# Kernel optimization log

Hardware: AMD Instinct MI355X
Metric: run time of the kernel (lower is better)

The kernel has to match this reference:

```python
import jax, jax.numpy as jnp
from jax import lax
import numpy as np

B, C, T = 512, 12, 4096
DS = 4          # int_downsize
STEPS = 7       # int_steps
KS = 51         # smooth_size
SIGMA = (KS - 1) // 2  # 25, per module: gaussian_filter1d(delta, smooth_centre)


def _gauss_kernel():
    # Replicates scipy.ndimage.gaussian_filter1d(delta, SIGMA) on a length-KS
    # delta array with default truncate=4.0 and mode='reflect'.
    r = int(4.0 * SIGMA + 0.5)
    x = np.arange(-r, r + 1)
    g = np.exp(-0.5 * (x / SIGMA) ** 2)
    g /= g.sum()
    delta = np.zeros(KS)
    delta[(KS - 1) // 2] = 1.0
    padded = np.pad(delta, r, mode='symmetric')  # scipy 'reflect' boundary
    filt = np.convolve(padded, g, mode='valid')  # len == KS (g is symmetric)
    return filt.astype(np.float32)


def resize_linear(x, factor):
    # F.interpolate(mode='linear', align_corners=False, recompute_scale_factor=False)
    Tin = x.shape[-1]
    Tout = int(Tin * factor)
    src = (jnp.arange(Tout, dtype=x.dtype) + 0.5) / factor - 0.5
    src = jnp.clip(src, 0.0, Tin - 1)
    i0 = jnp.floor(src).astype(jnp.int32)
    i1 = jnp.minimum(i0 + 1, Tin - 1)
    w = src - i0
    return x[..., i0] * (1.0 - w) + x[..., i1] * w


def resize_transform(x, factor):
    # ResizeTransformTime: resize the field AND rescale its magnitude
    if factor < 1:
        return factor * resize_linear(x, factor)
    elif factor > 1:
        return resize_linear(factor * x, factor)
    return x


def warp_1d(src, flow):
    # SpatialTransformer for 1D signals: torch fakes 2D grid_sample by repeating
    # src to [B,C,Tlen,2] and the grid to [B,1,Tlen,2]; with align_corners=True,
    # zeros padding, bilinear. The width-dim (size 2) interpolation collapses to a
    # scalar in-bounds weight xw since both width copies are identical.
    Tlen = src.shape[-1]
    new_locs = jnp.arange(Tlen, dtype=src.dtype) + flow          # [B,1,Tlen]
    v = 2.0 * (new_locs / (Tlen - 1) - 0.5)                      # normalized
    ix = (v + 1.0) * 0.5                                         # W=2 -> (W-1)=1
    iy = (v + 1.0) * 0.5 * (Tlen - 1)
    x0 = jnp.floor(ix)
    fx = ix - x0
    x0i = x0.astype(jnp.int32)
    xw = ((1.0 - fx) * ((x0i >= 0) & (x0i <= 1))
          + fx * ((x0i + 1 >= 0) & (x0i + 1 <= 1)))              # [B,1,Tlen]
    y0 = jnp.floor(iy)
    fy = iy - y0
    y0i = y0.astype(jnp.int32)
    y1i = y0i + 1
    vy0 = (y0i >= 0) & (y0i < Tlen)
    vy1 = (y1i >= 0) & (y1i < Tlen)
    y0c = jnp.clip(y0i, 0, Tlen - 1)
    y1c = jnp.clip(y1i, 0, Tlen - 1)
    Bc, Cc = src.shape[0], src.shape[1]
    idx0 = jnp.broadcast_to(y0c, (Bc, Cc, Tlen))
    idx1 = jnp.broadcast_to(y1c, (Bc, Cc, Tlen))
    g0 = jnp.take_along_axis(src, idx0, axis=-1)
    g1 = jnp.take_along_axis(src, idx1, axis=-1)
    return xw * ((1.0 - fy) * vy0 * g0 + fy * vy1 * g1)


def setup_inputs() -> dict:
    key = jax.random.key(0)
    k1, k2 = jax.random.split(key)
    source = jax.random.normal(k1, (B, C, T), dtype=jnp.float32)
    noise = jax.random.normal(k2, (B, 1, T), dtype=jnp.float32)
    flow_mag = jnp.ones((1,), dtype=jnp.float32)
    smooth_kernel = jnp.asarray(_gauss_kernel())
    return {"source": source, "flow_mag": flow_mag, "noise": noise,
            "smooth_kernel": smooth_kernel}


def reference(source, flow_mag, noise, smooth_kernel):
    flow_field = flow_mag * noise                      # [B,1,T]
    pos_flow = resize_transform(flow_field, 1.0 / DS)  # [B,1,T//DS]
    # VecInt: scaling and squaring
    vec = pos_flow * (1.0 / 2 ** STEPS)
    for _ in range(STEPS):
        vec = vec + warp_1d(vec, vec)
    pos_flow = resize_transform(vec, float(DS))        # back to [B,1,T]
    # conv1d smoothing (cross-correlation, same as F.conv1d)
    pad = (KS - 1) // 2
    pos_flow = lax.conv_general_dilated(
        pos_flow, smooth_kernel.reshape(1, 1, KS),
        window_strides=(1,), padding=[(pad, pad)],
        dimension_numbers=('NCH', 'OIH', 'NCH'))
    return warp_1d(source, pos_flow)
```

## Files before the change

kernel.cpp:

```cpp
#include <hip/hip_runtime.h>


#define BB 512
#define CC 12
#define TT 4096
#define TD 1024
#define KS 51
#define NT 1024

struct WarpW { int y0c, y1c; float w0, w1; };

template <int TLEN>
__device__ __forceinline__ WarpW warp_weights(int t, float flow) {
    const float tm1 = (float)(TLEN - 1);
    float nl = (float)t + flow;
    float v  = 2.0f * (nl / tm1 - 0.5f);
    float ix = (v + 1.0f) * 0.5f;
    float iy = ix * tm1;
    float x0 = floorf(ix);
    float fx = ix - x0;
    int   x0i = (int)x0;
    float m0 = (x0i >= 0 && x0i <= 1) ? 1.0f : 0.0f;
    float m1 = (x0i + 1 >= 0 && x0i + 1 <= 1) ? 1.0f : 0.0f;
    float xw = (1.0f - fx) * m0 + fx * m1;
    float y0 = floorf(iy);
    float fy = iy - y0;
    int   y0i = (int)y0;
    int   y1i = y0i + 1;
    float vy0 = (y0i >= 0 && y0i < TLEN) ? 1.0f : 0.0f;
    float vy1 = (y1i >= 0 && y1i < TLEN) ? 1.0f : 0.0f;
    WarpW r;
    r.y0c = min(max(y0i, 0), TLEN - 1);
    r.y1c = min(max(y1i, 0), TLEN - 1);
    r.w0 = xw * (1.0f - fy) * vy0;
    r.w1 = xw * fy * vy1;
    return r;
}

extern "C" __global__ void __launch_bounds__(NT)
rand_warp_aug_kernel(const float* __restrict__ source,
                     const float* __restrict__ flow_mag,
                     const float* __restrict__ noise,
                     const float* __restrict__ gk,
                     float* __restrict__ out) {
    __shared__ float vecA[TD];
    __shared__ float vecB[TD];
    __shared__ float pf_up[TT];
    __shared__ float g[KS];

    const int b   = blockIdx.x;
    const int tid = threadIdx.x;
    const float fm = flow_mag[0];

    const float* nrow = noise + (size_t)b * TT;
    if (tid < TD) {
        float x1 = fm * nrow[4 * tid + 1];
        float x2 = fm * nrow[4 * tid + 2];
        vecA[tid] = (x1 * 0.5f + x2 * 0.5f) * (0.25f * 0.0078125f);
    }
    if (tid < KS) g[tid] = gk[tid];
    __syncthreads();

    float* cur = vecA;
    float* nxt = vecB;
#pragma unroll 1
    for (int s = 0; s < 7; ++s) {
        if (tid < TD) {
            float fl = cur[tid];
            WarpW w = warp_weights<TD>(tid, fl);
            float g0 = cur[w.y0c];
            float g1 = cur[w.y1c];
            nxt[tid] = fl + (w.w0 * g0 + w.w1 * g1);
        }
        __syncthreads();
        float* tmp = cur; cur = nxt; nxt = tmp;
    }

#pragma unroll
    for (int jj = 0; jj < TT / NT; ++jj) {
        int j = tid + jj * NT;
        float srcp = ((float)j + 0.5f) * 0.25f - 0.5f;
        srcp = fminf(fmaxf(srcp, 0.0f), (float)(TD - 1));
        float flp = floorf(srcp);
        int   i0  = (int)flp;
        int   i1  = min(i0 + 1, TD - 1);
        float w   = srcp - flp;
        float a0  = 4.0f * cur[i0];
        float a1  = 4.0f * cur[i1];
        pf_up[j] = a0 * (1.0f - w) + a1 * w;
    }
    __syncthreads();

    const float* sbase = source + (size_t)b * CC * TT;
    float*       obase = out    + (size_t)b * CC * TT;
#pragma unroll 1
    for (int tt = 0; tt < TT / NT; ++tt) {
        int t = tid + tt * NT;
        float acc = 0.0f;
        int lo = t - (KS - 1) / 2;
#pragma unroll
        for (int k = 0; k < KS; ++k) {
            int idx = lo + k;
            float xv = (idx >= 0 && idx < TT) ? pf_up[idx] : 0.0f;
            acc += xv * g[k];
        }
        WarpW w = warp_weights<TT>(t, acc);
#pragma unroll
        for (int c = 0; c < CC; ++c) {
            const float* srow = sbase + (size_t)c * TT;
            float g0 = srow[w.y0c];
            float g1 = srow[w.y1c];
            obase[(size_t)c * TT + t] = w.w0 * g0 + w.w1 * g1;
        }
    }
}

extern "C" void kernel_launch(void* const* d_in, const int* in_sizes, int n_in,
                              void* d_out, int out_size, void* d_ws, size_t ws_size,
                              hipStream_t stream) {
    const float* source   = (const float*)d_in[0];
    const float* flow_mag = (const float*)d_in[1];
    const float* noise    = (const float*)d_in[2];
    const float* gk       = (const float*)d_in[3];
    float* out = (float*)d_out;

    rand_warp_aug_kernel<<<BB, NT, 0, stream>>>(source, flow_mag, noise, gk, out);
}
```

Measured before the change: 47.71 us.

## Split flow computation and source warp into separate kernels via workspace

Computes the smoothed flow field per batch row in one kernel and writes it to workspace. A second, fully parallel kernel with small blocks then performs the 12-channel gather warp. This decouples the serial scaling-and-squaring phase from the bandwidth-heavy gather, so the gather can fill the GPU with many blocks. It adds a workspace round trip for the flow field and a second launch, and falls back to the fused kernel if the workspace is too small.

```diff
diff --git a/kernel.cpp b/kernel.cpp
--- a/kernel.cpp
+++ b/kernel.cpp
@@ -7,6 +7,7 @@
 #define TD 1024
 #define KS 51
 #define NT 1024
+#define NT2 256
 
 struct WarpW { int y0c, y1c; float w0, w1; };
 
@@ -38,11 +39,10 @@
 }
 
 extern "C" __global__ void __launch_bounds__(NT)
-rand_warp_aug_kernel(const float* __restrict__ source,
-                     const float* __restrict__ flow_mag,
-                     const float* __restrict__ noise,
-                     const float* __restrict__ gk,
-                     float* __restrict__ out) {
+flow_kernel(const float* __restrict__ flow_mag,
+            const float* __restrict__ noise,
+            const float* __restrict__ gk,
+            float* __restrict__ pf_out) {
     __shared__ float vecA[TD];
     __shared__ float vecB[TD];
     __shared__ float pf_up[TT];
@@ -68,9 +68,7 @@
         if (tid < TD) {
             float fl = cur[tid];
             WarpW w = warp_weights<TD>(tid, fl);
-            float g0 = cur[w.y0c];
-            float g1 = cur[w.y1c];
-            nxt[tid] = fl + (w.w0 * g0 + w.w1 * g1);
+            nxt[tid] = fl + (w.w0 * cur[w.y0c] + w.w1 * cur[w.y1c]);
         }
         __syncthreads();
         float* tmp = cur; cur = nxt; nxt = tmp;
@@ -91,6 +89,96 @@
     }
     __syncthreads();
 
+    float* prow = pf_out + (size_t)b * TT;
+#pragma unroll
+    for (int tt = 0; tt < TT / NT; ++tt) {
+        int t = tid + tt * NT;
+        float acc = 0.0f;
+        int lo = t - (KS - 1) / 2;
+#pragma unroll
+        for (int k = 0; k < KS; ++k) {
+            int idx = lo + k;
+            float xv = (idx >= 0 && idx < TT) ? pf_up[idx] : 0.0f;
+            acc += xv * g[k];
+        }
+        prow[t] = acc;
+    }
+}
+
+extern "C" __global__ void __launch_bounds__(NT2)
+warp_kernel(const float* __restrict__ source,
+            const float* __restrict__ pf,
+            float* __restrict__ out) {
+    int gid = blockIdx.x * NT2 + threadIdx.x;
+    int b = gid >> 12;
+    int t = gid & (TT - 1);
+
+    float flow = pf[gid];
+    WarpW w = warp_weights<TT>(t, flow);
+
+    const float* sbase = source + (size_t)b * CC * TT;
+    float*       obase = out    + (size_t)b * CC * TT;
+#pragma unroll
+    for (int c = 0; c < CC; ++c) {
+        const float* srow = sbase + (size_t)c * TT;
+        float g0 = srow[w.y0c];
+        float g1 = srow[w.y1c];
+        obase[(size_t)c * TT + t] = w.w0 * g0 + w.w1 * g1;
+    }
+}
+
+extern "C" __global__ void __launch_bounds__(NT)
+rand_warp_aug_fused(const float* __restrict__ source,
+                    const float* __restrict__ flow_mag,
+                    const float* __restrict__ noise,
+                    const float* __restrict__ gk,
+                    float* __restrict__ out) {
+    __shared__ float vecA[TD];
+    __shared__ float vecB[TD];
+    __shared__ float pf_up[TT];
+    __shared__ float g[KS];
+
+    const int b   = blockIdx.x;
+    const int tid = threadIdx.x;
+    const float fm = flow_mag[0];
+
+    const float* nrow = noise + (size_t)b * TT;
+    if (tid < TD) {
+        float x1 = fm * nrow[4 * tid + 1];
+        float x2 = fm * nrow[4 * tid + 2];
+        vecA[tid] = (x1 * 0.5f + x2 * 0.5f) * (0.25f * 0.0078125f);
+    }
+    if (tid < KS) g[tid] = gk[tid];
+    __syncthreads();
+
+    float* cur = vecA;
+    float* nxt = vecB;
+#pragma unroll 1
+    for (int s = 0; s < 7; ++s) {
+        if (tid < TD) {
+            float fl = cur[tid];
+            WarpW w = warp_weights<TD>(tid, fl);
+            nxt[tid] = fl + (w.w0 * cur[w.y0c] + w.w1 * cur[w.y1c]);
+        }
+        __syncthreads();
+        float* tmp = cur; cur = nxt; nxt = tmp;
+    }
+
+#pragma unroll
+    for (int jj = 0; jj < TT / NT; ++jj) {
+        int j = tid + jj * NT;
+        float srcp = ((float)j + 0.5f) * 0.25f - 0.5f;
+        srcp = fminf(fmaxf(srcp, 0.0f), (float)(TD - 1));
+        float flp = floorf(srcp);
+        int   i0  = (int)flp;
+        int   i1  = min(i0 + 1, TD - 1);
+        float w   = srcp - flp;
+        float a0  = 4.0f * cur[i0];
+        float a1  = 4.0f * cur[i1];
+        pf_up[j] = a0 * (1.0f - w) + a1 * w;
+    }
+    __syncthreads();
+
     const float* sbase = source + (size_t)b * CC * TT;
     float*       obase = out    + (size_t)b * CC * TT;
 #pragma unroll 1
@@ -108,9 +196,7 @@
 #pragma unroll
         for (int c = 0; c < CC; ++c) {
             const float* srow = sbase + (size_t)c * TT;
-            float g0 = srow[w.y0c];
-            float g1 = srow[w.y1c];
-            obase[(size_t)c * TT + t] = w.w0 * g0 + w.w1 * g1;
+            obase[(size_t)c * TT + t] = w.w0 * srow[w.y0c] + w.w1 * srow[w.y1c];
         }
     }
 }
@@ -124,5 +210,12 @@
     const float* gk       = (const float*)d_in[3];
     float* out = (float*)d_out;
 
-    rand_warp_aug_kernel<<<BB, NT, 0, stream>>>(source, flow_mag, noise, gk, out);
-}
+    const size_t need = (size_t)BB * TT * sizeof(float);
+    if (ws_size >= need) {
+        float* pf = (float*)d_ws;
+        flow_kernel<<<BB, NT, 0, stream>>>(flow_mag, noise, gk, pf);
+        warp_kernel<<<(BB * TT) / NT2, NT2, 0, stream>>>(source, pf, out);
+    } else {
+        rand_warp_aug_fused<<<BB, NT, 0, stream>>>(source, flow_mag, noise, gk, out);
+    }
+}
```

After: 57.87 us. +21.3%, slower.

## Fold linear upsample into smoothing conv via precomputed polyphase weight table

Applied to the files above, without the earlier changes.

Composes the 4x linear upsampling and the 51-tap Gaussian into a 17-tap polyphase filter on the low-resolution field. The weights are precomputed per phase in shared memory, which removes the 4096-entry pf_up buffer, its barrier and the 51-tap loop per output. Boundary outputs fall back to a direct per-tap evaluation. Noise is now loaded with vector reads and the output loop is unrolled. The risks are small float differences from the changed summation order and some thread divergence in the boundary paths.

```diff
diff --git a/kernel.cpp b/kernel.cpp
--- a/kernel.cpp
+++ b/kernel.cpp
@@ -7,6 +7,12 @@
 #define TD 1024
 #define KS 51
 #define NT 1024
+#define NJ 17
+#define J0 (-8)
+#define T_LO 32
+#define T_HI 4063
+
+typedef float f32x4 __attribute__((ext_vector_type(4)));
 
 struct WarpW { int y0c, y1c; float w0, w1; };
 
@@ -37,6 +43,23 @@
     return r;
 }
 
+__device__ __forceinline__ float conv_direct(const float* __restrict__ vec,
+                                             const float* __restrict__ g, int t) {
+    float acc = 0.0f;
+    for (int k = 0; k < KS; ++k) {
+        int s = t + k - 25;
+        if (s < 0 || s >= TT) continue;
+        float srcp = 0.25f * (float)s - 0.375f;
+        srcp = fminf(fmaxf(srcp, 0.0f), (float)(TD - 1));
+        float flp = floorf(srcp);
+        int i0 = (int)flp;
+        int i1 = min(i0 + 1, TD - 1);
+        float w = srcp - flp;
+        acc += g[k] * 4.0f * ((1.0f - w) * vec[i0] + w * vec[i1]);
+    }
+    return acc;
+}
+
 extern "C" __global__ void __launch_bounds__(NT)
 rand_warp_aug_kernel(const float* __restrict__ source,
                      const float* __restrict__ flow_mag,
@@ -45,66 +68,80 @@
                      float* __restrict__ out) {
     __shared__ float vecA[TD];
     __shared__ float vecB[TD];
-    __shared__ float pf_up[TT];
     __shared__ float g[KS];
+    __shared__ float wtab[NJ][4];
 
     const int b   = blockIdx.x;
     const int tid = threadIdx.x;
     const float fm = flow_mag[0];
 
-    const float* nrow = noise + (size_t)b * TT;
-    if (tid < TD) {
-        float x1 = fm * nrow[4 * tid + 1];
-        float x2 = fm * nrow[4 * tid + 2];
+    const f32x4* nrow4 = (const f32x4*)(noise + (size_t)b * TT);
+    {
+        f32x4 nv = nrow4[tid];
+        float x1 = fm * nv.y;
+        float x2 = fm * nv.z;
         vecA[tid] = (x1 * 0.5f + x2 * 0.5f) * (0.25f * 0.0078125f);
     }
     if (tid < KS) g[tid] = gk[tid];
     __syncthreads();
 
+    if (tid < 4 * NJ) {
+        int p = tid / NJ;
+        int j = tid % NJ + J0;
+        float acc = 0.0f;
+        for (int k = 0; k < KS; ++k) {
+            int q = p + k - 25;
+            int d = (q >= 0) ? (q >> 2) : -((-q + 3) >> 2);
+            int r = q - 4 * d;
+            float c = 0.0f;
+            if (r == 0)      { if (j == d - 1) c = 0.375f; else if (j == d) c = 0.625f; }
+            else if (r == 1) { if (j == d - 1) c = 0.125f; else if (j == d) c = 0.875f; }
+            else if (r == 2) { if (j == d)     c = 0.875f; else if (j == d + 1) c = 0.125f; }
+            else             { if (j == d)     c = 0.625f; else if (j == d + 1) c = 0.375f; }
+            acc += g[k] * c;
+        }
+        wtab[tid % NJ][p] = 4.0f * acc;
+    }
+
     float* cur = vecA;
     float* nxt = vecB;
 #pragma unroll 1
     for (int s = 0; s < 7; ++s) {
-        if (tid < TD) {
+        {
             float fl = cur[tid];
             WarpW w = warp_weights<TD>(tid, fl);
-            float g0 = cur[w.y0c];
-            float g1 = cur[w.y1c];
-            nxt[tid] = fl + (w.w0 * g0 + w.w1 * g1);
+            nxt[tid] = fl + (w.w0 * cur[w.y0c] + w.w1 * cur[w.y1c]);
         }
         __syncthreads();
         float* tmp = cur; cur = nxt; nxt = tmp;
     }
 
+    const int p  = tid & 3;
+    const int Tb = tid >> 2;
+    float pf[4];
+    {
+        float wreg;
+        float a0 = 0.0f, a1 = 0.0f, a2 = 0.0f, a3 = 0.0f;
 #pragma unroll
-    for (int jj = 0; jj < TT / NT; ++jj) {
-        int j = tid + jj * NT;
-        float srcp = ((float)j + 0.5f) * 0.25f - 0.5f;
-        srcp = fminf(fmaxf(srcp, 0.0f), (float)(TD - 1));
-        float flp = floorf(srcp);
-        int   i0  = (int)flp;
-        int   i1  = min(i0 + 1, TD - 1);
-        float w   = srcp - flp;
-        float a0  = 4.0f * cur[i0];
-        float a1  = 4.0f * cur[i1];
-        pf_up[j] = a0 * (1.0f - w) + a1 * w;
+        for (int j = 0; j < NJ; ++j) {
+            wreg = wtab[j][p];
+            int base = Tb + j + J0;
+            a0 += wreg * cur[base];
+            a1 += wreg * cur[base + 256];
+            a2 += wreg * cur[base + 512];
+            a3 += wreg * cur[base + 768];
+        }
+        pf[0] = a0; pf[1] = a1; pf[2] = a2; pf[3] = a3;
     }
-    __syncthreads();
+    if (tid < T_LO)            pf[0] = conv_direct(cur, g, tid);
+    if (tid >= NT - (TT - 1 - T_HI)) pf[3] = conv_direct(cur, g, tid + 3 * NT);
 
     const float* sbase = source + (size_t)b * CC * TT;
     float*       obase = out    + (size_t)b * CC * TT;
-#pragma unroll 1
+#pragma unroll
     for (int tt = 0; tt < TT / NT; ++tt) {
         int t = tid + tt * NT;
-        float acc = 0.0f;
-        int lo = t - (KS - 1) / 2;
-#pragma unroll
-        for (int k = 0; k < KS; ++k) {
-            int idx = lo + k;
-            float xv = (idx >= 0 && idx < TT) ? pf_up[idx] : 0.0f;
-            acc += xv * g[k];
-        }
-        WarpW w = warp_weights<TT>(t, acc);
+        WarpW w = warp_weights<TT>(t, pf[tt]);
 #pragma unroll
         for (int c = 0; c < CC; ++c) {
             const float* srow = sbase + (size_t)c * TT;
```

Result: slower. 55.40 us (+16.1%).
